# Performance work log

Hardware: AMD Instinct MI355X
Metric: run time of the kernel (lower is better)

Reference implementation:

```python
import jax, jax.numpy as jnp
import numpy as np

EPS = 1e-6      # NMF denominator epsilon (Hamburger NMF2D)
LN_EPS = 1e-5   # torch LayerNorm default eps
STEPS = 6      # number_of_iterations
R = 64          # NMF rank (upstream MD_R default)


def _nmf_local_step(xm, bases, coef):
    # xm: (B, D, N); bases: (B, D, R); coef: (B, N, R)
    num = jnp.einsum('bdn,bdr->bnr', xm, bases)
    btb = jnp.einsum('bdr,bds->brs', bases, bases)
    coef = coef * num / (jnp.einsum('bnr,brs->bns', coef, btb) + EPS)
    num = jnp.einsum('bdn,bnr->bdr', xm, coef)
    ctc = jnp.einsum('bnr,bns->brs', coef, coef)
    bases = bases * num / (jnp.einsum('bdr,brs->bds', bases, ctc) + EPS)
    return bases, coef


def nmf2d(xm, bases0, steps):
    # xm: (B, D, N) nonnegative; bases0: (1, D, R) fixed buffer (RAND_INIT=False)
    B = xm.shape[0]
    xs = jax.lax.stop_gradient(xm)  # local_inference runs under torch.no_grad()
    bases = jnp.broadcast_to(bases0, (B,) + bases0.shape[1:])
    coef = jax.nn.softmax(jnp.einsum('bdn,bdr->bnr', xs, bases), axis=-1)  # inv_t = 1 for NMF

    def body(i, carry):
        b, c = carry
        return _nmf_local_step(xs, b, c)

    bases, coef = jax.lax.fori_loop(0, steps, body, (bases, coef))
    bases = jax.lax.stop_gradient(bases)
    coef = jax.lax.stop_gradient(coef)
    # compute_coef: one multiplicative coef update WITH gradients w.r.t. xm
    num = jnp.einsum('bdn,bdr->bnr', xm, bases)
    btb = jnp.einsum('bdr,bds->brs', bases, bases)
    coef = coef * num / (jnp.einsum('bnr,brs->bns', coef, btb) + EPS)
    # reconstruct: (B, D, R) @ (B, R, N) -> (B, D, N)
    return jnp.einsum('bdr,bnr->bdn', bases, coef)


def setup_inputs() -> dict:
    key = jax.random.key(0)
    ks = jax.random.split(key, 4)
    B, S, F, FFN = 8, 1024, 1024, 4096
    Nc = FFN // 2
    x = jax.random.normal(ks[0], (B, S, F), jnp.float32)
    U_w = jax.random.normal(ks[1], (FFN, F), jnp.float32) / np.sqrt(F).astype(np.float32)
    U_b = jnp.zeros((FFN,), jnp.float32)
    ln_g = jnp.ones((Nc,), jnp.float32)
    ln_b = jnp.zeros((Nc,), jnp.float32)
    bases = jax.random.uniform(ks[2], (1, S, R), jnp.float32)
    bases = bases / (jnp.linalg.norm(bases, axis=1, keepdims=True) + 1e-12)  # F.normalize(dim=1)
    V_w = jax.random.normal(ks[3], (F, Nc), jnp.float32) / np.sqrt(Nc).astype(np.float32)
    V_b = jnp.zeros((F,), jnp.float32)
    return dict(x=x, U_w=U_w, U_b=U_b, ln_g=ln_g, ln_b=ln_b, bases=bases, V_w=V_w, V_b=V_b)


def reference(x, U_w, U_b, ln_g, ln_b, bases, V_w, V_b):
    # x: (B, S, F)
    h = jax.nn.gelu(x @ U_w.T + U_b, approximate=False)  # (B, S, FFN)
    z1, z2 = jnp.split(h, 2, axis=-1)                    # each (B, S, FFN//2)
    mu = z2.mean(-1, keepdims=True)
    var = z2.var(-1, keepdims=True)
    z2 = (z2 - mu) / jnp.sqrt(var + LN_EPS) * ln_g + ln_b
    xm = jax.nn.relu(z2)             # (B, D=S, N=FFN//2), matches NMF2D spatial view
    z2 = nmf2d(xm, bases, STEPS)     # (B, S, FFN//2)
    return (z1 * z2) @ V_w.T + V_b   # (B, S, F)
```

## Files before the change

kernel.cpp:

```cpp
#include <hip/hip_runtime.h>
#include <math.h>


typedef __bf16 bf16;
typedef bf16 bf16x4 __attribute__((ext_vector_type(4)));
typedef bf16 bf16x8 __attribute__((ext_vector_type(8)));
typedef float f32x4 __attribute__((ext_vector_type(4)));

#define NMF_EPS 1e-6f
#define LNEPS   1e-5f
#define NKS     8

#if defined(__has_builtin)
#if __has_builtin(__builtin_amdgcn_global_load_lds)
#define HAS_GLL 1
#endif
#endif

__device__ __forceinline__ void split2(float x, bf16& h, bf16& l) {
    h = (bf16)x;
    l = (bf16)(x - (float)h);
}

__global__ __launch_bounds__(256) void detect_dtype(const void* x, int* flag) {
    __shared__ int bad_sh;
    if (threadIdx.x == 0) bad_sh = 0;
    __syncthreads();
    const bf16* p = (const bf16*)x;
    int bad = 0;
    for (int i = threadIdx.x; i < 1024; i += 256) {
        float f = (float)p[i];
        if (!(fabsf(f) < 1000.f)) bad = 1;
    }
    if (bad) atomicOr(&bad_sh, 1);
    __syncthreads();
    if (threadIdx.x == 0) *flag = bad_sh;
}

__global__ __launch_bounds__(256)
void conv_all(const void* s0, const void* s1, const void* s2, const void* s3,
              const void* s4, const void* s5, const void* s6, const void* s7,
              bf16* __restrict__ ar, const int* __restrict__ flag) {
    const int is_f32 = *flag;
    const int total4 = 3688704;
    for (int i = blockIdx.x * 256 + threadIdx.x; i < total4; i += gridDim.x * 256) {
        const void* src; int loc; size_t doff;
        if (i < 2097152)      { src = s0; loc = i;           doff = 0; }
        else if (i < 3145728) { src = s1; loc = i - 2097152; doff = 8388608; }
        else if (i < 3146752) { src = s2; loc = i - 3145728; doff = 12582912; }
        else if (i < 3147264) { src = s3; loc = i - 3146752; doff = 12587008; }
        else if (i < 3147776) { src = s4; loc = i - 3147264; doff = 12589056; }
        else if (i < 3164160) { src = s5; loc = i - 3147776; doff = 12591104; }
        else if (i < 3688448) { src = s6; loc = i - 3164160; doff = 12656640; }
        else                  { src = s7; loc = i - 3688448; doff = 14753792; }
        bf16x4 o;
        if (is_f32) {
            f32x4 v = ((const f32x4*)src)[loc];
            o[0] = (bf16)v[0]; o[1] = (bf16)v[1]; o[2] = (bf16)v[2]; o[3] = (bf16)v[3];
        } else {
            o = ((const bf16x4*)src)[loc];
        }
        *(bf16x4*)(ar + doff + (size_t)loc * 4) = o;
    }
}

template <int EPI>
__global__ __launch_bounds__(256)
void gemm_bt(const bf16* __restrict__ A, const bf16* __restrict__ B,
             const bf16* __restrict__ bias,
             bf16* __restrict__ o0, bf16* __restrict__ o1,
             float* __restrict__ outf, bf16* __restrict__ outb,
             int K, int N, const int* __restrict__ flag) {
    __shared__ bf16 As[128 * 32];
    __shared__ bf16 Bs[128 * 32];
    const int tid = threadIdx.x;
    const int bm = blockIdx.x, bn = blockIdx.y;
    const bf16* Ab = A + (size_t)bm * 128 * K;
    const bf16* Bb = B + (size_t)bn * 128 * K;
    const int w = tid >> 6, lane = tid & 63, lm = lane & 15, lq = lane >> 4;
    const int m_off = (w >> 1) * 64, n_off = (w & 1) * 64;
    const int of32 = (EPI == 1) ? *flag : 0;
    f32x4 acc[4][4];
#pragma unroll
    for (int i = 0; i < 4; i++)
#pragma unroll
        for (int j = 0; j < 4; j++) { acc[i][j][0]=0.f; acc[i][j][1]=0.f; acc[i][j][2]=0.f; acc[i][j][3]=0.f; }

    const int r0 = tid * 8;
    const int row0 = r0 >> 5, col0 = r0 & 31;
    const int wb = w * 512;
    for (int k0 = 0; k0 < K; k0 += 32) {
        __syncthreads();
        const bf16* gA0 = Ab + (size_t)row0 * K        + k0 + col0;
        const bf16* gA1 = Ab + (size_t)(row0 + 64) * K + k0 + col0;
        const bf16* gB0 = Bb + (size_t)row0 * K        + k0 + col0;
        const bf16* gB1 = Bb + (size_t)(row0 + 64) * K + k0 + col0;
#ifdef HAS_GLL
        __builtin_amdgcn_global_load_lds((const __attribute__((address_space(1))) void*)gA0,
                                         (__attribute__((address_space(3))) void*)&As[wb], 16, 0, 0);
        __builtin_amdgcn_global_load_lds((const __attribute__((address_space(1))) void*)gA1,
                                         (__attribute__((address_space(3))) void*)&As[wb + 2048], 16, 0, 0);
        __builtin_amdgcn_global_load_lds((const __attribute__((address_space(1))) void*)gB0,
                                         (__attribute__((address_space(3))) void*)&Bs[wb], 16, 0, 0);
        __builtin_amdgcn_global_load_lds((const __attribute__((address_space(1))) void*)gB1,
                                         (__attribute__((address_space(3))) void*)&Bs[wb + 2048], 16, 0, 0);
#else
        *(int4*)(&As[r0])        = *(const int4*)gA0;
        *(int4*)(&As[r0 + 2048]) = *(const int4*)gA1;
        *(int4*)(&Bs[r0])        = *(const int4*)gB0;
        *(int4*)(&Bs[r0 + 2048]) = *(const int4*)gB1;
#endif
        __syncthreads();
        bf16x8 af[4], bg[4];
#pragma unroll
        for (int i = 0; i < 4; i++) af[i] = *(const bf16x8*)&As[(m_off + i * 16 + lm) * 32 + lq * 8];
#pragma unroll
        for (int j = 0; j < 4; j++) bg[j] = *(const bf16x8*)&Bs[(n_off + j * 16 + lm) * 32 + lq * 8];
#pragma unroll
        for (int i = 0; i < 4; i++)
#pragma unroll
            for (int j = 0; j < 4; j++)
                acc[i][j] = __builtin_amdgcn_mfma_f32_16x16x32_bf16(af[i], bg[j], acc[i][j], 0, 0, 0);
    }
    const int gm0 = bm * 128 + m_off, gn0 = bn * 128 + n_off;
#pragma unroll
    for (int i = 0; i < 4; i++) {
#pragma unroll
        for (int j = 0; j < 4; j++) {
            const int gn = gn0 + j * 16 + lm;
            const float bv = (float)bias[gn];
#pragma unroll
            for (int e = 0; e < 4; e++) {
                const int gm = gm0 + i * 16 + lq * 4 + e;
                float v = acc[i][j][e] + bv;
                if (EPI == 0) {
                    v = 0.5f * v * (1.f + erff(v * 0.70710678118654752f));
                    if (gn < 2048) o0[(size_t)gm * 2048 + gn] = (bf16)v;
                    else           o1[(size_t)gm * 2048 + (gn - 2048)] = (bf16)v;
                } else {
                    if (of32) outf[(size_t)gm * N + gn] = v;
                    else      outb[(size_t)gm * N + gn] = (bf16)v;
                }
            }
        }
    }
}

__global__ __launch_bounds__(256)
void ln_relu(bf16* __restrict__ z, const bf16* __restrict__ g, const bf16* __restrict__ b) {
    const int row = blockIdx.x;
    bf16* zr = z + (size_t)row * 2048;
    const int t = threadIdx.x;
    bf16x4 a0 = *(bf16x4*)(zr + t * 4);
    bf16x4 a1 = *(bf16x4*)(zr + 1024 + t * 4);
    float v0[4], v1[4];
#pragma unroll
    for (int i = 0; i < 4; i++) { v0[i] = (float)a0[i]; v1[i] = (float)a1[i]; }
    float s = 0.f, q = 0.f;
#pragma unroll
    for (int i = 0; i < 4; i++) { s += v0[i] + v1[i]; q += v0[i] * v0[i] + v1[i] * v1[i]; }
#pragma unroll
    for (int off = 32; off >= 1; off >>= 1) { s += __shfl_down(s, off); q += __shfl_down(q, off); }
    __shared__ float red[8];
    __shared__ float mv[2];
    const int wv = t >> 6;
    if ((t & 63) == 0) { red[wv] = s; red[4 + wv] = q; }
    __syncthreads();
    if (t == 0) {
        float S = red[0] + red[1] + red[2] + red[3];
        float Q = red[4] + red[5] + red[6] + red[7];
        float mu = S * (1.f / 2048.f);
        float var = Q * (1.f / 2048.f) - mu * mu;
        mv[0] = mu; mv[1] = rsqrtf(var + LNEPS);
    }
    __syncthreads();
    const float mu = mv[0], ri = mv[1];
#pragma unroll
    for (int i = 0; i < 4; i++) {
        int c0 = t * 4 + i, c1 = 1024 + t * 4 + i;
        a0[i] = (bf16)fmaxf((v0[i] - mu) * ri * (float)g[c0] + (float)b[c0], 0.f);
        a1[i] = (bf16)fmaxf((v1[i] - mu) * ri * (float)g[c1] + (float)b[c1], 0.f);
    }
    *(bf16x4*)(zr + t * 4) = a0;
    *(bf16x4*)(zr + 1024 + t * 4) = a1;
}

__global__ __launch_bounds__(256)
void transpose_xm(const bf16* __restrict__ src, bf16* __restrict__ dst) {
    const int n0 = blockIdx.x * 64, d0 = blockIdx.y * 64, b = blockIdx.z;
    const bf16* S = src + (size_t)b * 1024 * 2048;
    bf16* Dst = dst + (size_t)b * 2048 * 1024;
    __shared__ bf16 tl[64 * 72];
    const int t = threadIdx.x;
    const int tr = t >> 2, tc = (t & 3) * 16;
    bf16x8 v0 = *(const bf16x8*)(S + (size_t)(d0 + tr) * 2048 + n0 + tc);
    bf16x8 v1 = *(const bf16x8*)(S + (size_t)(d0 + tr) * 2048 + n0 + tc + 8);
    *(bf16x8*)&tl[tr * 72 + tc] = v0;
    *(bf16x8*)&tl[tr * 72 + tc + 8] = v1;
    __syncthreads();
    bf16 o[16];
#pragma unroll
    for (int i = 0; i < 16; i++) o[i] = tl[(tc + i) * 72 + tr];
    *(bf16x8*)(Dst + (size_t)(n0 + tr) * 1024 + d0 + tc) = *(bf16x8*)&o[0];
    *(bf16x8*)(Dst + (size_t)(n0 + tr) * 1024 + d0 + tc + 8) = *(bf16x8*)&o[8];
}

__global__ __launch_bounds__(256)
void bases_init2(const bf16* __restrict__ b0, float* __restrict__ bases,
                 bf16* __restrict__ bNh, bf16* __restrict__ bNl,
                 bf16* __restrict__ bTh, bf16* __restrict__ bTl) {
    const int d0 = blockIdx.x * 64, b = blockIdx.y;
    __shared__ bf16 tl[64 * 72];
    const int t = threadIdx.x;
    const int tr = t >> 2, tc = (t & 3) * 16;
    bf16x8 v0 = *(const bf16x8*)(b0 + (size_t)(d0 + tr) * 64 + tc);
    bf16x8 v1 = *(const bf16x8*)(b0 + (size_t)(d0 + tr) * 64 + tc + 8);
    *(bf16x8*)&tl[tr * 72 + tc] = v0;
    *(bf16x8*)&tl[tr * 72 + tc + 8] = v1;
    bf16x8 zz;
#pragma unroll
    for (int i = 0; i < 8; i++) zz[i] = (bf16)0.f;
    f32x4 f0, f1, f2, f3;
#pragma unroll
    for (int i = 0; i < 4; i++) { f0[i]=(float)v0[i]; f1[i]=(float)v0[i+4]; f2[i]=(float)v1[i]; f3[i]=(float)v1[i+4]; }
    const size_t nb = (size_t)b * 1024 * 64 + (size_t)(d0 + tr) * 64 + tc;
    *(f32x4*)(bases + nb)      = f0;
    *(f32x4*)(bases + nb + 4)  = f1;
    *(f32x4*)(bases + nb + 8)  = f2;
    *(f32x4*)(bases + nb + 12) = f3;
    *(bf16x8*)(bNh + nb)     = v0;
    *(bf16x8*)(bNh + nb + 8) = v1;
    *(bf16x8*)(bNl + nb)     = zz;
    *(bf16x8*)(bNl + nb + 8) = zz;
    __syncthreads();
    bf16 o[16];
#pragma unroll
    for (int i = 0; i < 16; i++) o[i] = tl[(tc + i) * 72 + tr];
    const size_t tb = (size_t)b * 64 * 1024 + (size_t)tr * 1024 + d0 + tc;
    *(bf16x8*)(bTh + tb)     = *(bf16x8*)&o[0];
    *(bf16x8*)(bTh + tb + 8) = *(bf16x8*)&o[8];
    *(bf16x8*)(bTl + tb)     = zz;
    *(bf16x8*)(bTl + tb + 8) = zz;
}

__global__ __launch_bounds__(256)
void gram64p(const bf16* __restrict__ Th, const bf16* __restrict__ Tl,
             int K, float* __restrict__ Gp) {
    const int ks = blockIdx.x, b = blockIdx.y;
    const int KC = K / NKS;
    const int kbeg = ks * KC, kend = kbeg + KC;
    const bf16* H = Th + (size_t)b * 64 * K;
    const bf16* L = Tl + (size_t)b * 64 * K;
    __shared__ bf16 Hs[64 * 40], Ls[64 * 40];
    const int t = threadIdx.x, lane = t & 63, w = t >> 6;
    const int lm = lane & 15, lq = lane >> 4;
    const int srow = t >> 2, scol = (t & 3) * 8;
    f32x4 acc[4];
#pragma unroll
    for (int j = 0; j < 4; j++) { acc[j][0]=0.f; acc[j][1]=0.f; acc[j][2]=0.f; acc[j][3]=0.f; }
    for (int k0 = kbeg; k0 < kend; k0 += 32) {
        __syncthreads();
        *(int4*)&Hs[srow * 40 + scol] = *(const int4*)(H + (size_t)srow * K + k0 + scol);
        *(int4*)&Ls[srow * 40 + scol] = *(const int4*)(L + (size_t)srow * K + k0 + scol);
        __syncthreads();
        bf16x8 aH = *(const bf16x8*)&Hs[(w * 16 + lm) * 40 + lq * 8];
        bf16x8 aL = *(const bf16x8*)&Ls[(w * 16 + lm) * 40 + lq * 8];
#pragma unroll
        for (int j = 0; j < 4; j++) {
            bf16x8 bH = *(const bf16x8*)&Hs[(j * 16 + lm) * 40 + lq * 8];
            bf16x8 bL = *(const bf16x8*)&Ls[(j * 16 + lm) * 40 + lq * 8];
            acc[j] = __builtin_amdgcn_mfma_f32_16x16x32_bf16(aH, bH, acc[j], 0, 0, 0);
            acc[j] = __builtin_amdgcn_mfma_f32_16x16x32_bf16(aH, bL, acc[j], 0, 0, 0);
            acc[j] = __builtin_amdgcn_mfma_f32_16x16x32_bf16(aL, bH, acc[j], 0, 0, 0);
        }
    }
    float* Gb = Gp + ((size_t)b * NKS + ks) * 4096;
#pragma unroll
    for (int j = 0; j < 4; j++)
#pragma unroll
        for (int e = 0; e < 4; e++)
            Gb[(w * 16 + lq * 4 + e) * 64 + j * 16 + lm] = acc[j][e];
}

template <int MODE>
__global__ __launch_bounds__(256)
void coef_step(const bf16* __restrict__ xmT, const bf16* __restrict__ bTh,
               const bf16* __restrict__ bTl, const float* __restrict__ btb,
               float* __restrict__ coef,
               bf16* __restrict__ cNh, bf16* __restrict__ cNl,
               bf16* __restrict__ cTh, bf16* __restrict__ cTl) {
    const int n0 = blockIdx.x * 64, b = blockIdx.y;
    const bf16* X = xmT + (size_t)b * 2048 * 1024 + (size_t)n0 * 1024;
    const bf16* H = bTh + (size_t)b * 64 * 1024;
    const bf16* L = bTl + (size_t)b * 64 * 1024;
    __shared__ bf16 xs[64 * 40], hs[64 * 40], ls[64 * 40];
    __shared__ float cold[(MODE == 1) ? 64 * 65 : 1];
    __shared__ float gsm[(MODE == 1) ? 64 * 64 : 1];
    const int t = threadIdx.x;
    float* Cb = coef + (size_t)b * 2048 * 64 + (size_t)n0 * 64;
    if constexpr (MODE == 1) {
        const int rr = t >> 2, cc = (t & 3) * 16;
#pragma unroll
        for (int i = 0; i < 4; i++)
            *(f32x4*)&cold[rr * 65 + cc + i * 4] = *(const f32x4*)(Cb + (size_t)rr * 64 + cc + i * 4);
        const float* Gb = btb + (size_t)b * NKS * 4096;
#pragma unroll
        for (int i = 0; i < 4; i++) {
            f32x4 s4; s4[0]=0.f; s4[1]=0.f; s4[2]=0.f; s4[3]=0.f;
#pragma unroll
            for (int ks = 0; ks < NKS; ks++)
                s4 += *(const f32x4*)(Gb + ks * 4096 + rr * 64 + cc + i * 4);
            *(f32x4*)&gsm[rr * 64 + cc + i * 4] = s4;
        }
    }
    const int lane = t & 63, w = t >> 6, lm = lane & 15, lq = lane >> 4;
    const int srow = t >> 2, scol = (t & 3) * 8;
    f32x4 acc[4];
#pragma unroll
    for (int j = 0; j < 4; j++) { acc[j][0]=0.f; acc[j][1]=0.f; acc[j][2]=0.f; acc[j][3]=0.f; }
    for (int k0 = 0; k0 < 1024; k0 += 32) {
        __syncthreads();
        *(int4*)&xs[srow * 40 + scol] = *(const int4*)(X + (size_t)srow * 1024 + k0 + scol);
        *(int4*)&hs[srow * 40 + scol] = *(const int4*)(H + (size_t)srow * 1024 + k0 + scol);
        *(int4*)&ls[srow * 40 + scol] = *(const int4*)(L + (size_t)srow * 1024 + k0 + scol);
        __syncthreads();
        bf16x8 a = *(const bf16x8*)&xs[(w * 16 + lm) * 40 + lq * 8];
#pragma unroll
        for (int j = 0; j < 4; j++) {
            bf16x8 bh = *(const bf16x8*)&hs[(j * 16 + lm) * 40 + lq * 8];
            bf16x8 bl = *(const bf16x8*)&ls[(j * 16 + lm) * 40 + lq * 8];
            acc[j] = __builtin_amdgcn_mfma_f32_16x16x32_bf16(a, bh, acc[j], 0, 0, 0);
            acc[j] = __builtin_amdgcn_mfma_f32_16x16x32_bf16(a, bl, acc[j], 0, 0, 0);
        }
    }
    const int nbase = w * 16 + lq * 4;
    float out[4][4];
    if constexpr (MODE == 0) {
#pragma unroll
        for (int e = 0; e < 4; e++) {
            float m = fmaxf(fmaxf(acc[0][e], acc[1][e]), fmaxf(acc[2][e], acc[3][e]));
#pragma unroll
            for (int off = 1; off < 16; off <<= 1) m = fmaxf(m, __shfl_xor(m, off));
            float ex[4], s = 0.f;
#pragma unroll
            for (int j = 0; j < 4; j++) { ex[j] = expf(acc[j][e] - m); s += ex[j]; }
#pragma unroll
            for (int off = 1; off < 16; off <<= 1) s += __shfl_xor(s, off);
            const float inv = 1.f / s;
#pragma unroll
            for (int j = 0; j < 4; j++) out[j][e] = ex[j] * inv;
        }
    } else {
        float den[4][4];
#pragma unroll
        for (int j = 0; j < 4; j++)
#pragma unroll
            for (int e = 0; e < 4; e++) den[j][e] = 0.f;
#pragma unroll 8
        for (int s = 0; s < 64; s++) {
            float g4[4], c4[4];
#pragma unroll
            for (int j = 0; j < 4; j++) g4[j] = gsm[s * 64 + j * 16 + lm];
#pragma unroll
            for (int e = 0; e < 4; e++) c4[e] = cold[(nbase + e) * 65 + s];
#pragma unroll
            for (int j = 0; j < 4; j++)
#pragma unroll
                for (int e = 0; e < 4; e++) den[j][e] += c4[e] * g4[j];
        }
#pragma unroll
        for (int j = 0; j < 4; j++)
#pragma unroll
            for (int e = 0; e < 4; e++)
                out[j][e] = cold[(nbase + e) * 65 + j * 16 + lm] * acc[j][e] / (den[j][e] + NMF_EPS);
    }
#pragma unroll
    for (int j = 0; j < 4; j++) {
        const int r = j * 16 + lm;
#pragma unroll
        for (int e = 0; e < 4; e++) {
            const int nl = nbase + e;
            Cb[(size_t)nl * 64 + r] = out[j][e];
            if constexpr (MODE == 1) {
                bf16 h, l2;
                split2(out[j][e], h, l2);
                cNh[(size_t)b * 2048 * 64 + (size_t)(n0 + nl) * 64 + r] = h;
                cNl[(size_t)b * 2048 * 64 + (size_t)(n0 + nl) * 64 + r] = l2;
            }
        }
    }
    if constexpr (MODE == 1) {
        __syncthreads();
#pragma unroll
        for (int j = 0; j < 4; j++)
#pragma unroll
            for (int e = 0; e < 4; e++)
                cold[(j * 16 + lm) * 65 + nbase + e] = out[j][e];
        __syncthreads();
        const int rr = t >> 2, nc = (t & 3) * 16;
        bf16 hh[16], ll2[16];
#pragma unroll
        for (int i = 0; i < 16; i++) split2(cold[rr * 65 + nc + i], hh[i], ll2[i]);
        const size_t tb = (size_t)b * 64 * 2048 + (size_t)rr * 2048 + n0 + nc;
        *(bf16x8*)(cTh + tb)     = *(bf16x8*)&hh[0];
        *(bf16x8*)(cTh + tb + 8) = *(bf16x8*)&hh[8];
        *(bf16x8*)(cTl + tb)     = *(bf16x8*)&ll2[0];
        *(bf16x8*)(cTl + tb + 8) = *(bf16x8*)&ll2[8];
    }
}

__global__ __launch_bounds__(256)
void bases_step(const bf16* __restrict__ xm, const bf16* __restrict__ cTh,
                const bf16* __restrict__ cTl, const float* __restrict__ ctc,
                float* __restrict__ bases,
                bf16* __restrict__ bNh, bf16* __restrict__ bNl,
                bf16* __restrict__ bTh, bf16* __restrict__ bTl) {
    const int d0 = blockIdx.x * 32, b = blockIdx.y;
    const bf16* X = xm + (size_t)b * 1024 * 2048 + (size_t)d0 * 2048;
    const bf16* H = cTh + (size_t)b * 64 * 2048;
    const bf16* L = cTl + (size_t)b * 64 * 2048;
    __shared__ bf16 hs[64 * 40], ls[64 * 40], xds[32 * 40];
    __shared__ float bold[32 * 65];
    __shared__ float gsm[64 * 64];
    const int t = threadIdx.x;
    float* Bb = bases + (size_t)b * 1024 * 64 + (size_t)d0 * 64;
    {
        const int rr = t >> 3, cc = (t & 7) * 8;
        *(f32x4*)&bold[rr * 65 + cc]     = *(const f32x4*)(Bb + (size_t)rr * 64 + cc);
        *(f32x4*)&bold[rr * 65 + cc + 4] = *(const f32x4*)(Bb + (size_t)rr * 64 + cc + 4);
        const int r2 = t >> 2, c2 = (t & 3) * 16;
        const float* Gb = ctc + (size_t)b * NKS * 4096;
#pragma unroll
        for (int i = 0; i < 4; i++) {
            f32x4 s4; s4[0]=0.f; s4[1]=0.f; s4[2]=0.f; s4[3]=0.f;
#pragma unroll
            for (int ks = 0; ks < NKS; ks++)
                s4 += *(const f32x4*)(Gb + ks * 4096 + r2 * 64 + c2 + i * 4);
            *(f32x4*)&gsm[r2 * 64 + c2 + i * 4] = s4;
        }
    }
    const int lane = t & 63, w = t >> 6, lm = lane & 15, lq = lane >> 4;
    const int srow = t >> 2, scol = (t & 3) * 8;
    f32x4 acc[2];
#pragma unroll
    for (int j = 0; j < 2; j++) { acc[j][0]=0.f; acc[j][1]=0.f; acc[j][2]=0.f; acc[j][3]=0.f; }
    for (int k0 = 0; k0 < 2048; k0 += 32) {
        __syncthreads();
        *(int4*)&hs[srow * 40 + scol] = *(const int4*)(H + (size_t)srow * 2048 + k0 + scol);
        *(int4*)&ls[srow * 40 + scol] = *(const int4*)(L + (size_t)srow * 2048 + k0 + scol);
        if (t < 128) {
            const int xr = t >> 2, xc2 = (t & 3) * 8;
            *(int4*)&xds[xr * 40 + xc2] = *(const int4*)(X + (size_t)xr * 2048 + k0 + xc2);
        }
        __syncthreads();
        bf16x8 ah = *(const bf16x8*)&hs[(w * 16 + lm) * 40 + lq * 8];
        bf16x8 al = *(const bf16x8*)&ls[(w * 16 + lm) * 40 + lq * 8];
#pragma unroll
        for (int j = 0; j < 2; j++) {
            bf16x8 bx = *(const bf16x8*)&xds[(j * 16 + lm) * 40 + lq * 8];
            acc[j] = __builtin_amdgcn_mfma_f32_16x16x32_bf16(ah, bx, acc[j], 0, 0, 0);
            acc[j] = __builtin_amdgcn_mfma_f32_16x16x32_bf16(al, bx, acc[j], 0, 0, 0);
        }
    }
    const int rbase = w * 16 + lq * 4;
    float den[2][4];
#pragma unroll
    for (int j = 0; j < 2; j++)
#pragma unroll
        for (int e = 0; e < 4; e++) den[j][e] = 0.f;
#pragma unroll 8
    for (int s = 0; s < 64; s++) {
        float g4[4], b2[2];
#pragma unroll
        for (int e = 0; e < 4; e++) g4[e] = gsm[s * 64 + rbase + e];
#pragma unroll
        for (int j = 0; j < 2; j++) b2[j] = bold[(j * 16 + lm) * 65 + s];
#pragma unroll
        for (int j = 0; j < 2; j++)
#pragma unroll
            for (int e = 0; e < 4; e++) den[j][e] += b2[j] * g4[e];
    }
    float out[2][4];
#pragma unroll
    for (int j = 0; j < 2; j++)
#pragma unroll
        for (int e = 0; e < 4; e++)
            out[j][e] = bold[(j * 16 + lm) * 65 + rbase + e] * acc[j][e] / (den[j][e] + NMF_EPS);
    __syncthreads();
#pragma unroll
    for (int j = 0; j < 2; j++)
#pragma unroll
        for (int e = 0; e < 4; e++)
            bold[(j * 16 + lm) * 65 + rbase + e] = out[j][e];
    __syncthreads();
    {
        const int dd = t >> 3, rc = (t & 7) * 8;
        float v[8];
#pragma unroll
        for (int i = 0; i < 8; i++) v[i] = bold[dd * 65 + rc + i];
        *(f32x4*)(Bb + (size_t)dd * 64 + rc)     = *(f32x4*)&v[0];
        *(f32x4*)(Bb + (size_t)dd * 64 + rc + 4) = *(f32x4*)&v[4];
        bf16 hv[8], lv[8];
#pragma unroll
        for (int i = 0; i < 8; i++) split2(v[i], hv[i], lv[i]);
        const size_t nb = (size_t)b * 1024 * 64 + (size_t)(d0 + dd) * 64 + rc;
        *(bf16x8*)(bNh + nb) = *(bf16x8*)&hv[0];
        *(bf16x8*)(bNl + nb) = *(bf16x8*)&lv[0];
    }
    {
        const int rr = t >> 2, dc = (t & 3) * 8;
        bf16 hv[8], lv[8];
#pragma unroll
        for (int i = 0; i < 8; i++) split2(bold[(dc + i) * 65 + rr], hv[i], lv[i]);
        const size_t tb = (size_t)b * 64 * 1024 + (size_t)rr * 1024 + d0 + dc;
        *(bf16x8*)(bTh + tb) = *(bf16x8*)&hv[0];
        *(bf16x8*)(bTl + tb) = *(bf16x8*)&lv[0];
    }
}

__global__ __launch_bounds__(256)
void recon_gate2(bf16* __restrict__ z1A, const bf16* __restrict__ bNh,
                 const bf16* __restrict__ bNl, const bf16* __restrict__ cNh,
                 const bf16* __restrict__ cNl) {
    const int n0 = blockIdx.x * 128, s0 = blockIdx.y * 128, b = blockIdx.z;
    const bf16* Ah = bNh + (size_t)b * 1024 * 64 + (size_t)s0 * 64;
    const bf16* Al = bNl + (size_t)b * 1024 * 64 + (size_t)s0 * 64;
    const bf16* Bh = cNh + (size_t)b * 2048 * 64 + (size_t)n0 * 64;
    const bf16* Bl = cNl + (size_t)b * 2048 * 64 + (size_t)n0 * 64;
    __shared__ bf16 ahs[128 * 72], als[128 * 72], bhs[128 * 72], bls[128 * 72];
    const int t = threadIdx.x;
#pragma unroll
    for (int i = 0; i < 4; i++) {
        const int idx = t * 4 + i;
        const int r_ = idx >> 3, c_ = (idx & 7) * 8;
        *(int4*)&ahs[r_ * 72 + c_] = *(const int4*)(Ah + (size_t)r_ * 64 + c_);
        *(int4*)&als[r_ * 72 + c_] = *(const int4*)(Al + (size_t)r_ * 64 + c_);
        *(int4*)&bhs[r_ * 72 + c_] = *(const int4*)(Bh + (size_t)r_ * 64 + c_);
        *(int4*)&bls[r_ * 72 + c_] = *(const int4*)(Bl + (size_t)r_ * 64 + c_);
    }
    __syncthreads();
    const int lane = t & 63, w = t >> 6, lm = lane & 15, lq = lane >> 4;
    const int m_off = (w >> 1) * 64, n_off = (w & 1) * 64;
    f32x4 acc[4][4];
#pragma unroll
    for (int i = 0; i < 4; i++)
#pragma unroll
        for (int j = 0; j < 4; j++) { acc[i][j][0]=0.f; acc[i][j][1]=0.f; acc[i][j][2]=0.f; acc[i][j][3]=0.f; }
#pragma unroll
    for (int kk = 0; kk < 2; kk++) {
        bf16x8 afh[4], afl[4], bgh[4], bgl[4];
#pragma unroll
        for (int i = 0; i < 4; i++) {
            afh[i] = *(const bf16x8*)&ahs[(m_off + i * 16 + lm) * 72 + kk * 32 + lq * 8];
            afl[i] = *(const bf16x8*)&als[(m_off + i * 16 + lm) * 72 + kk * 32 + lq * 8];
        }
#pragma unroll
        for (int j = 0; j < 4; j++) {
            bgh[j] = *(const bf16x8*)&bhs[(n_off + j * 16 + lm) * 72 + kk * 32 + lq * 8];
            bgl[j] = *(const bf16x8*)&bls[(n_off + j * 16 + lm) * 72 + kk * 32 + lq * 8];
        }
#pragma unroll
        for (int i = 0; i < 4; i++)
#pragma unroll
            for (int j = 0; j < 4; j++) {
                acc[i][j] = __builtin_amdgcn_mfma_f32_16x16x32_bf16(afh[i], bgh[j], acc[i][j], 0, 0, 0);
                acc[i][j] = __builtin_amdgcn_mfma_f32_16x16x32_bf16(afh[i], bgl[j], acc[i][j], 0, 0, 0);
                acc[i][j] = __builtin_amdgcn_mfma_f32_16x16x32_bf16(afl[i], bgh[j], acc[i][j], 0, 0, 0);
            }
    }
    bf16* Z = z1A + ((size_t)b * 1024 + s0) * 2048 + n0;
#pragma unroll
    for (int i = 0; i < 4; i++)
#pragma unroll
        for (int j = 0; j < 4; j++) {
            const int gn = n_off + j * 16 + lm;
#pragma unroll
            for (int e = 0; e < 4; e++) {
                const int gm = m_off + i * 16 + lq * 4 + e;
                bf16* p = Z + (size_t)gm * 2048 + gn;
                *p = (bf16)((float)*p * acc[i][j][e]);
            }
        }
}

extern "C" void kernel_launch(void* const* d_in, const int* in_sizes, int n_in,
                              void* d_out, int out_size, void* d_ws, size_t ws_size,
                              hipStream_t stream) {
    (void)in_sizes; (void)n_in; (void)out_size; (void)ws_size;
    char* ws = (char*)d_ws;
    bf16*  z1A   = (bf16*)(ws);
    bf16*  xmB   = (bf16*)(ws + 33554432);
    bf16*  xmT   = (bf16*)(ws + 67108864);
    char*  ar    = ws + 100663296;
    bf16* xc   = (bf16*)(ar);
    bf16* Uwc  = (bf16*)(ar + 16777216);
    bf16* Ubc  = (bf16*)(ar + 25165824);
    bf16* lngc = (bf16*)(ar + 25174016);
    bf16* lnbc = (bf16*)(ar + 25178112);
    bf16* b0c  = (bf16*)(ar + 25182208);
    bf16* Vwc  = (bf16*)(ar + 25313280);
    bf16* Vbc  = (bf16*)(ar + 29507584);
    int*  dflag = (int*)(ar + 29509632);
    float* bases = (float*)(ar);
    float* coef  = (float*)(ar + 2097152);
    bf16* bTh = (bf16*)(ar + 6291456);
    bf16* bTl = (bf16*)(ar + 7340032);
    bf16* bNh = (bf16*)(ar + 8388608);
    bf16* bNl = (bf16*)(ar + 9437184);
    bf16* cTh = (bf16*)(ar + 10485760);
    bf16* cTl = (bf16*)(ar + 12582912);
    bf16* cNh = (bf16*)(ar + 14680064);
    bf16* cNl = (bf16*)(ar + 16777216);
    float* btb = (float*)(ar + 18874368);
    float* ctc = (float*)(ar + 19922944);

    detect_dtype<<<1, 256, 0, stream>>>(d_in[0], dflag);
    conv_all<<<dim3(2048), 256, 0, stream>>>(d_in[0], d_in[1], d_in[2], d_in[3],
                                             d_in[4], d_in[5], d_in[6], d_in[7],
                                             (bf16*)ar, dflag);

    gemm_bt<0><<<dim3(64, 32), 256, 0, stream>>>(xc, Uwc, Ubc, z1A, xmB,
                                                 nullptr, nullptr, 1024, 4096, nullptr);
    ln_relu<<<dim3(8192), 256, 0, stream>>>(xmB, lngc, lnbc);
    transpose_xm<<<dim3(32, 16, 8), 256, 0, stream>>>(xmB, xmT);
    bases_init2<<<dim3(16, 8), 256, 0, stream>>>(b0c, bases, bNh, bNl, bTh, bTl);
    coef_step<0><<<dim3(32, 8), 256, 0, stream>>>(xmT, bTh, bTl, nullptr, coef,
                                                  nullptr, nullptr, nullptr, nullptr);
    for (int it = 0; it < 7; ++it) {
        gram64p<<<dim3(NKS, 8), 256, 0, stream>>>(bTh, bTl, 1024, btb);
        coef_step<1><<<dim3(32, 8), 256, 0, stream>>>(xmT, bTh, bTl, btb, coef,
                                                      cNh, cNl, cTh, cTl);
        if (it < 6) {
            gram64p<<<dim3(NKS, 8), 256, 0, stream>>>(cTh, cTl, 2048, ctc);
            bases_step<<<dim3(32, 8), 256, 0, stream>>>(xmB, cTh, cTl, ctc, bases,
                                                        bNh, bNl, bTh, bTl);
        }
    }
    recon_gate2<<<dim3(16, 8, 8), 256, 0, stream>>>(z1A, bNh, bNl, cNh, cNl);
    gemm_bt<1><<<dim3(64, 8), 256, 0, stream>>>(z1A, Vwc, Vbc, nullptr, nullptr,
                                                (float*)d_out, (bf16*)d_out,
                                                2048, 1024, dflag);
}
```

Baseline: 877.5 us.

## Double-buffer LDS with register prefetch and K=64 tiles in NMF step kernels

The coef_step and bases_step kernels now use double-buffered shared memory tiles of depth 64 instead of 32. The next tile's global loads are issued into registers before the current tile's MFMAs and stored to the alternate buffer afterwards, so each iteration needs one barrier instead of two. This aims to hide global-load latency behind MFMA work and halve the loop-iteration and sync overhead. In exchange it uses more LDS and registers, which may lower occupancy.

Result: faster. 775.0 us (-11.7%).

```diff
diff --git a/kernel.cpp b/kernel.cpp
--- a/kernel.cpp
+++ b/kernel.cpp
@@ -293,7 +293,7 @@
     const bf16* X = xmT + (size_t)b * 2048 * 1024 + (size_t)n0 * 1024;
     const bf16* H = bTh + (size_t)b * 64 * 1024;
     const bf16* L = bTl + (size_t)b * 64 * 1024;
-    __shared__ bf16 xs[64 * 40], hs[64 * 40], ls[64 * 40];
+    __shared__ bf16 xs[2][64 * 72], hs[2][64 * 72], ls[2][64 * 72];
     __shared__ float cold[(MODE == 1) ? 64 * 65 : 1];
     __shared__ float gsm[(MODE == 1) ? 64 * 64 : 1];
     const int t = threadIdx.x;
@@ -314,24 +314,62 @@
         }
     }
     const int lane = t & 63, w = t >> 6, lm = lane & 15, lq = lane >> 4;
-    const int srow = t >> 2, scol = (t & 3) * 8;
+    const int srow = t >> 2, scol = (t & 3) * 16;
+    int4 rx0, rx1, rh0, rh1, rl0, rl1;
+    {
+        rx0 = *(const int4*)(X + (size_t)srow * 1024 + scol);
+        rx1 = *(const int4*)(X + (size_t)srow * 1024 + scol + 8);
+        rh0 = *(const int4*)(H + (size_t)srow * 1024 + scol);
+        rh1 = *(const int4*)(H + (size_t)srow * 1024 + scol + 8);
+        rl0 = *(const int4*)(L + (size_t)srow * 1024 + scol);
+        rl1 = *(const int4*)(L + (size_t)srow * 1024 + scol + 8);
+        bf16* xb = &xs[0][srow * 72 + scol];
+        bf16* hb = &hs[0][srow * 72 + scol];
+        bf16* lb = &ls[0][srow * 72 + scol];
+        *(int4*)xb = rx0; *(int4*)(xb + 8) = rx1;
+        *(int4*)hb = rh0; *(int4*)(hb + 8) = rh1;
+        *(int4*)lb = rl0; *(int4*)(lb + 8) = rl1;
+    }
+    __syncthreads();
     f32x4 acc[4];
 #pragma unroll
     for (int j = 0; j < 4; j++) { acc[j][0]=0.f; acc[j][1]=0.f; acc[j][2]=0.f; acc[j][3]=0.f; }
-    for (int k0 = 0; k0 < 1024; k0 += 32) {
+    int cur = 0;
+    for (int kt = 0; kt < 16; kt++) {
+        if (kt < 15) {
+            const int k0 = (kt + 1) * 64;
+            rx0 = *(const int4*)(X + (size_t)srow * 1024 + k0 + scol);
+            rx1 = *(const int4*)(X + (size_t)srow * 1024 + k0 + scol + 8);
+            rh0 = *(const int4*)(H + (size_t)srow * 1024 + k0 + scol);
+            rh1 = *(const int4*)(H + (size_t)srow * 1024 + k0 + scol + 8);
+            rl0 = *(const int4*)(L + (size_t)srow * 1024 + k0 + scol);
+            rl1 = *(const int4*)(L + (size_t)srow * 1024 + k0 + scol + 8);
+        }
+        {
+            bf16x8 a0 = *(const bf16x8*)&xs[cur][(w * 16 + lm) * 72 + lq * 8];
+            bf16x8 a1 = *(const bf16x8*)&xs[cur][(w * 16 + lm) * 72 + 32 + lq * 8];
+#pragma unroll
+            for (int j = 0; j < 4; j++) {
+                bf16x8 bh0 = *(const bf16x8*)&hs[cur][(j * 16 + lm) * 72 + lq * 8];
+                bf16x8 bl0 = *(const bf16x8*)&ls[cur][(j * 16 + lm) * 72 + lq * 8];
+                acc[j] = __builtin_amdgcn_mfma_f32_16x16x32_bf16(a0, bh0, acc[j], 0, 0, 0);
+                acc[j] = __builtin_amdgcn_mfma_f32_16x16x32_bf16(a0, bl0, acc[j], 0, 0, 0);
+                bf16x8 bh1 = *(const bf16x8*)&hs[cur][(j * 16 + lm) * 72 + 32 + lq * 8];
+                bf16x8 bl1 = *(const bf16x8*)&ls[cur][(j * 16 + lm) * 72 + 32 + lq * 8];
+                acc[j] = __builtin_amdgcn_mfma_f32_16x16x32_bf16(a1, bh1, acc[j], 0, 0, 0);
+                acc[j] = __builtin_amdgcn_mfma_f32_16x16x32_bf16(a1, bl1, acc[j], 0, 0, 0);
+            }
+        }
+        if (kt < 15) {
+            bf16* xb = &xs[cur ^ 1][srow * 72 + scol];
+            bf16* hb = &hs[cur ^ 1][srow * 72 + scol];
+            bf16* lb = &ls[cur ^ 1][srow * 72 + scol];
+            *(int4*)xb = rx0; *(int4*)(xb + 8) = rx1;
+            *(int4*)hb = rh0; *(int4*)(hb + 8) = rh1;
+            *(int4*)lb = rl0; *(int4*)(lb + 8) = rl1;
+        }
         __syncthreads();
-        *(int4*)&xs[srow * 40 + scol] = *(const int4*)(X + (size_t)srow * 1024 + k0 + scol);
-        *(int4*)&hs[srow * 40 + scol] = *(const int4*)(H + (size_t)srow * 1024 + k0 + scol);
-        *(int4*)&ls[srow * 40 + scol] = *(const int4*)(L + (size_t)srow * 1024 + k0 + scol);
-        __syncthreads();
-        bf16x8 a = *(const bf16x8*)&xs[(w * 16 + lm) * 40 + lq * 8];
-#pragma unroll
-        for (int j = 0; j < 4; j++) {
-            bf16x8 bh = *(const bf16x8*)&hs[(j * 16 + lm) * 40 + lq * 8];
-            bf16x8 bl = *(const bf16x8*)&ls[(j * 16 + lm) * 40 + lq * 8];
-            acc[j] = __builtin_amdgcn_mfma_f32_16x16x32_bf16(a, bh, acc[j], 0, 0, 0);
-            acc[j] = __builtin_amdgcn_mfma_f32_16x16x32_bf16(a, bl, acc[j], 0, 0, 0);
-        }
+        cur ^= 1;
     }
     const int nbase = w * 16 + lq * 4;
     float out[4][4];
@@ -419,7 +457,7 @@
     const bf16* X = xm + (size_t)b * 1024 * 2048 + (size_t)d0 * 2048;
     const bf16* H = cTh + (size_t)b * 64 * 2048;
     const bf16* L = cTl + (size_t)b * 64 * 2048;
-    __shared__ bf16 hs[64 * 40], ls[64 * 40], xds[32 * 40];
+    __shared__ bf16 hs[2][64 * 72], ls[2][64 * 72], xds[2][32 * 72];
     __shared__ float bold[32 * 65];
     __shared__ float gsm[64 * 64];
     const int t = threadIdx.x;
@@ -440,27 +478,59 @@
         }
     }
     const int lane = t & 63, w = t >> 6, lm = lane & 15, lq = lane >> 4;
-    const int srow = t >> 2, scol = (t & 3) * 8;
+    const int srow = t >> 2, scol = (t & 3) * 16;
+    const int xrow = t >> 3, xcol = (t & 7) * 8;
+    int4 rh0, rh1, rl0, rl1, rxd;
+    {
+        rh0 = *(const int4*)(H + (size_t)srow * 2048 + scol);
+        rh1 = *(const int4*)(H + (size_t)srow * 2048 + scol + 8);
+        rl0 = *(const int4*)(L + (size_t)srow * 2048 + scol);
+        rl1 = *(const int4*)(L + (size_t)srow * 2048 + scol + 8);
+        rxd = *(const int4*)(X + (size_t)xrow * 2048 + xcol);
+        bf16* hb = &hs[0][srow * 72 + scol];
+        bf16* lb = &ls[0][srow * 72 + scol];
+        *(int4*)hb = rh0; *(int4*)(hb + 8) = rh1;
+        *(int4*)lb = rl0; *(int4*)(lb + 8) = rl1;
+        *(int4*)&xds[0][xrow * 72 + xcol] = rxd;
+    }
+    __syncthreads();
     f32x4 acc[2];
 #pragma unroll
     for (int j = 0; j < 2; j++) { acc[j][0]=0.f; acc[j][1]=0.f; acc[j][2]=0.f; acc[j][3]=0.f; }
-    for (int k0 = 0; k0 < 2048; k0 += 32) {
+    int cur = 0;
+    for (int kt = 0; kt < 32; kt++) {
+        if (kt < 31) {
+            const int k0 = (kt + 1) * 64;
+            rh0 = *(const int4*)(H + (size_t)srow * 2048 + k0 + scol);
+            rh1 = *(const int4*)(H + (size_t)srow * 2048 + k0 + scol + 8);
+            rl0 = *(const int4*)(L + (size_t)srow * 2048 + k0 + scol);
+            rl1 = *(const int4*)(L + (size_t)srow * 2048 + k0 + scol + 8);
+            rxd = *(const int4*)(X + (size_t)xrow * 2048 + k0 + xcol);
+        }
+        {
+            bf16x8 ah0 = *(const bf16x8*)&hs[cur][(w * 16 + lm) * 72 + lq * 8];
+            bf16x8 al0 = *(const bf16x8*)&ls[cur][(w * 16 + lm) * 72 + lq * 8];
+            bf16x8 ah1 = *(const bf16x8*)&hs[cur][(w * 16 + lm) * 72 + 32 + lq * 8];
+            bf16x8 al1 = *(const bf16x8*)&ls[cur][(w * 16 + lm) * 72 + 32 + lq * 8];
+#pragma unroll
+            for (int j = 0; j < 2; j++) {
+                bf16x8 bx0 = *(const bf16x8*)&xds[cur][(j * 16 + lm) * 72 + lq * 8];
+                acc[j] = __builtin_amdgcn_mfma_f32_16x16x32_bf16(ah0, bx0, acc[j], 0, 0, 0);
+                acc[j] = __builtin_amdgcn_mfma_f32_16x16x32_bf16(al0, bx0, acc[j], 0, 0, 0);
+                bf16x8 bx1 = *(const bf16x8*)&xds[cur][(j * 16 + lm) * 72 + 32 + lq * 8];
+                acc[j] = __builtin_amdgcn_mfma_f32_16x16x32_bf16(ah1, bx1, acc[j], 0, 0, 0);
+                acc[j] = __builtin_amdgcn_mfma_f32_16x16x32_bf16(al1, bx1, acc[j], 0, 0, 0);
+            }
+        }
+        if (kt < 31) {
+            bf16* hb = &hs[cur ^ 1][srow * 72 + scol];
+            bf16* lb = &ls[cur ^ 1][srow * 72 + scol];
+            *(int4*)hb = rh0; *(int4*)(hb + 8) = rh1;
+            *(int4*)lb = rl0; *(int4*)(lb + 8) = rl1;
+            *(int4*)&xds[cur ^ 1][xrow * 72 + xcol] = rxd;
+        }
         __syncthreads();
-        *(int4*)&hs[srow * 40 + scol] = *(const int4*)(H + (size_t)srow * 2048 + k0 + scol);
-        *(int4*)&ls[srow * 40 + scol] = *(const int4*)(L + (size_t)srow * 2048 + k0 + scol);
-        if (t < 128) {
-            const int xr = t >> 2, xc2 = (t & 3) * 8;
-            *(int4*)&xds[xr * 40 + xc2] = *(const int4*)(X + (size_t)xr * 2048 + k0 + xc2);
-        }
-        __syncthreads();
-        bf16x8 ah = *(const bf16x8*)&hs[(w * 16 + lm) * 40 + lq * 8];
-        bf16x8 al = *(const bf16x8*)&ls[(w * 16 + lm) * 40 + lq * 8];
-#pragma unroll
-        for (int j = 0; j < 2; j++) {
-            bf16x8 bx = *(const bf16x8*)&xds[(j * 16 + lm) * 40 + lq * 8];
-            acc[j] = __builtin_amdgcn_mfma_f32_16x16x32_bf16(ah, bx, acc[j], 0, 0, 0);
-            acc[j] = __builtin_amdgcn_mfma_f32_16x16x32_bf16(al, bx, acc[j], 0, 0, 0);
-        }
+        cur ^= 1;
     }
     const int rbase = w * 16 + lq * 4;
     float den[2][4];
```

## Load NMF MFMA operands directly from global memory, drop LDS staging

Applied to the files above, without the earlier changes.

The gram, coef and bases step kernels no longer stage tiles through shared memory behind paired barriers. Each lane now loads its MFMA fragments straight from global memory, and the inner loops are unrolled to process 64 K-elements per iteration. The gram partial split count is raised from 8 to 16 for more blocks, and the ctc buffer offset moves to make room for the larger partial buffer. This removes per-tile syncs and LDS traffic, but it relies on cache hits for B operands that are re-read across warps and accepts less coalesced global access.

Measured after the change: 1.054 ms. +20.1%, slower.

```diff
diff --git a/kernel.cpp b/kernel.cpp
--- a/kernel.cpp
+++ b/kernel.cpp
@@ -9,7 +9,7 @@
 
 #define NMF_EPS 1e-6f
 #define LNEPS   1e-5f
-#define NKS     8
+#define NKS     16
 
 #if defined(__has_builtin)
 #if __has_builtin(__builtin_amdgcn_global_load_lds)
@@ -251,24 +251,22 @@
     const int kbeg = ks * KC, kend = kbeg + KC;
     const bf16* H = Th + (size_t)b * 64 * K;
     const bf16* L = Tl + (size_t)b * 64 * K;
-    __shared__ bf16 Hs[64 * 40], Ls[64 * 40];
     const int t = threadIdx.x, lane = t & 63, w = t >> 6;
     const int lm = lane & 15, lq = lane >> 4;
-    const int srow = t >> 2, scol = (t & 3) * 8;
+    const bf16* Ha = H + (size_t)(w * 16 + lm) * K + lq * 8;
+    const bf16* La = L + (size_t)(w * 16 + lm) * K + lq * 8;
+    const bf16* Hb = H + (size_t)lm * K + lq * 8;
+    const bf16* Lb = L + (size_t)lm * K + lq * 8;
     f32x4 acc[4];
 #pragma unroll
     for (int j = 0; j < 4; j++) { acc[j][0]=0.f; acc[j][1]=0.f; acc[j][2]=0.f; acc[j][3]=0.f; }
     for (int k0 = kbeg; k0 < kend; k0 += 32) {
-        __syncthreads();
-        *(int4*)&Hs[srow * 40 + scol] = *(const int4*)(H + (size_t)srow * K + k0 + scol);
-        *(int4*)&Ls[srow * 40 + scol] = *(const int4*)(L + (size_t)srow * K + k0 + scol);
-        __syncthreads();
-        bf16x8 aH = *(const bf16x8*)&Hs[(w * 16 + lm) * 40 + lq * 8];
-        bf16x8 aL = *(const bf16x8*)&Ls[(w * 16 + lm) * 40 + lq * 8];
+        bf16x8 aH = *(const bf16x8*)(Ha + k0);
+        bf16x8 aL = *(const bf16x8*)(La + k0);
 #pragma unroll
         for (int j = 0; j < 4; j++) {
-            bf16x8 bH = *(const bf16x8*)&Hs[(j * 16 + lm) * 40 + lq * 8];
-            bf16x8 bL = *(const bf16x8*)&Ls[(j * 16 + lm) * 40 + lq * 8];
+            bf16x8 bH = *(const bf16x8*)(Hb + (size_t)j * 16 * K + k0);
+            bf16x8 bL = *(const bf16x8*)(Lb + (size_t)j * 16 * K + k0);
             acc[j] = __builtin_amdgcn_mfma_f32_16x16x32_bf16(aH, bH, acc[j], 0, 0, 0);
             acc[j] = __builtin_amdgcn_mfma_f32_16x16x32_bf16(aH, bL, acc[j], 0, 0, 0);
             acc[j] = __builtin_amdgcn_mfma_f32_16x16x32_bf16(aL, bH, acc[j], 0, 0, 0);
@@ -293,7 +291,6 @@
     const bf16* X = xmT + (size_t)b * 2048 * 1024 + (size_t)n0 * 1024;
     const bf16* H = bTh + (size_t)b * 64 * 1024;
     const bf16* L = bTl + (size_t)b * 64 * 1024;
-    __shared__ bf16 xs[64 * 40], hs[64 * 40], ls[64 * 40];
     __shared__ float cold[(MODE == 1) ? 64 * 65 : 1];
     __shared__ float gsm[(MODE == 1) ? 64 * 64 : 1];
     const int t = threadIdx.x;
@@ -314,25 +311,29 @@
         }
     }
     const int lane = t & 63, w = t >> 6, lm = lane & 15, lq = lane >> 4;
-    const int srow = t >> 2, scol = (t & 3) * 8;
+    const bf16* Xr = X + (size_t)(w * 16 + lm) * 1024 + lq * 8;
+    const bf16* Hr = H + (size_t)lm * 1024 + lq * 8;
+    const bf16* Lr = L + (size_t)lm * 1024 + lq * 8;
     f32x4 acc[4];
 #pragma unroll
     for (int j = 0; j < 4; j++) { acc[j][0]=0.f; acc[j][1]=0.f; acc[j][2]=0.f; acc[j][3]=0.f; }
-    for (int k0 = 0; k0 < 1024; k0 += 32) {
-        __syncthreads();
-        *(int4*)&xs[srow * 40 + scol] = *(const int4*)(X + (size_t)srow * 1024 + k0 + scol);
-        *(int4*)&hs[srow * 40 + scol] = *(const int4*)(H + (size_t)srow * 1024 + k0 + scol);
-        *(int4*)&ls[srow * 40 + scol] = *(const int4*)(L + (size_t)srow * 1024 + k0 + scol);
-        __syncthreads();
-        bf16x8 a = *(const bf16x8*)&xs[(w * 16 + lm) * 40 + lq * 8];
+#pragma unroll 2
+    for (int k0 = 0; k0 < 1024; k0 += 64) {
+        bf16x8 a0 = *(const bf16x8*)(Xr + k0);
+        bf16x8 a1 = *(const bf16x8*)(Xr + k0 + 32);
 #pragma unroll
         for (int j = 0; j < 4; j++) {
-            bf16x8 bh = *(const bf16x8*)&hs[(j * 16 + lm) * 40 + lq * 8];
-            bf16x8 bl = *(const bf16x8*)&ls[(j * 16 + lm) * 40 + lq * 8];
-            acc[j] = __builtin_amdgcn_mfma_f32_16x16x32_bf16(a, bh, acc[j], 0, 0, 0);
-            acc[j] = __builtin_amdgcn_mfma_f32_16x16x32_bf16(a, bl, acc[j], 0, 0, 0);
-        }
-    }
+            bf16x8 bh0 = *(const bf16x8*)(Hr + (size_t)j * 16 * 1024 + k0);
+            bf16x8 bl0 = *(const bf16x8*)(Lr + (size_t)j * 16 * 1024 + k0);
+            acc[j] = __builtin_amdgcn_mfma_f32_16x16x32_bf16(a0, bh0, acc[j], 0, 0, 0);
+            acc[j] = __builtin_amdgcn_mfma_f32_16x16x32_bf16(a0, bl0, acc[j], 0, 0, 0);
+            bf16x8 bh1 = *(const bf16x8*)(Hr + (size_t)j * 16 * 1024 + k0 + 32);
+            bf16x8 bl1 = *(const bf16x8*)(Lr + (size_t)j * 16 * 1024 + k0 + 32);
+            acc[j] = __builtin_amdgcn_mfma_f32_16x16x32_bf16(a1, bh1, acc[j], 0, 0, 0);
+            acc[j] = __builtin_amdgcn_mfma_f32_16x16x32_bf16(a1, bl1, acc[j], 0, 0, 0);
+        }
+    }
+    if constexpr (MODE == 1) __syncthreads();
     const int nbase = w * 16 + lq * 4;
     float out[4][4];
     if constexpr (MODE == 0) {
@@ -419,7 +420,6 @@
     const bf16* X = xm + (size_t)b * 1024 * 2048 + (size_t)d0 * 2048;
     const bf16* H = cTh + (size_t)b * 64 * 2048;
     const bf16* L = cTl + (size_t)b * 64 * 2048;
-    __shared__ bf16 hs[64 * 40], ls[64 * 40], xds[32 * 40];
     __shared__ float bold[32 * 65];
     __shared__ float gsm[64 * 64];
     const int t = threadIdx.x;
@@ -440,28 +440,29 @@
         }
     }
     const int lane = t & 63, w = t >> 6, lm = lane & 15, lq = lane >> 4;
-    const int srow = t >> 2, scol = (t & 3) * 8;
+    const bf16* Hr = H + (size_t)(w * 16 + lm) * 2048 + lq * 8;
+    const bf16* Lr = L + (size_t)(w * 16 + lm) * 2048 + lq * 8;
+    const bf16* Xr = X + (size_t)lm * 2048 + lq * 8;
     f32x4 acc[2];
 #pragma unroll
     for (int j = 0; j < 2; j++) { acc[j][0]=0.f; acc[j][1]=0.f; acc[j][2]=0.f; acc[j][3]=0.f; }
-    for (int k0 = 0; k0 < 2048; k0 += 32) {
-        __syncthreads();
-        *(int4*)&hs[srow * 40 + scol] = *(const int4*)(H + (size_t)srow * 2048 + k0 + scol);
-        *(int4*)&ls[srow * 40 + scol] = *(const int4*)(L + (size_t)srow * 2048 + k0 + scol);
-        if (t < 128) {
-            const int xr = t >> 2, xc2 = (t & 3) * 8;
-            *(int4*)&xds[xr * 40 + xc2] = *(const int4*)(X + (size_t)xr * 2048 + k0 + xc2);
-        }
-        __syncthreads();
-        bf16x8 ah = *(const bf16x8*)&hs[(w * 16 + lm) * 40 + lq * 8];
-        bf16x8 al = *(const bf16x8*)&ls[(w * 16 + lm) * 40 + lq * 8];
+#pragma unroll 2
+    for (int k0 = 0; k0 < 2048; k0 += 64) {
+        bf16x8 ah0 = *(const bf16x8*)(Hr + k0);
+        bf16x8 al0 = *(const bf16x8*)(Lr + k0);
+        bf16x8 ah1 = *(const bf16x8*)(Hr + k0 + 32);
+        bf16x8 al1 = *(const bf16x8*)(Lr + k0 + 32);
 #pragma unroll
         for (int j = 0; j < 2; j++) {
-            bf16x8 bx = *(const bf16x8*)&xds[(j * 16 + lm) * 40 + lq * 8];
-            acc[j] = __builtin_amdgcn_mfma_f32_16x16x32_bf16(ah, bx, acc[j], 0, 0, 0);
-            acc[j] = __builtin_amdgcn_mfma_f32_16x16x32_bf16(al, bx, acc[j], 0, 0, 0);
-        }
-    }
+            bf16x8 bx0 = *(const bf16x8*)(Xr + (size_t)j * 16 * 2048 + k0);
+            acc[j] = __builtin_amdgcn_mfma_f32_16x16x32_bf16(ah0, bx0, acc[j], 0, 0, 0);
+            acc[j] = __builtin_amdgcn_mfma_f32_16x16x32_bf16(al0, bx0, acc[j], 0, 0, 0);
+            bf16x8 bx1 = *(const bf16x8*)(Xr + (size_t)j * 16 * 2048 + k0 + 32);
+            acc[j] = __builtin_amdgcn_mfma_f32_16x16x32_bf16(ah1, bx1, acc[j], 0, 0, 0);
+            acc[j] = __builtin_amdgcn_mfma_f32_16x16x32_bf16(al1, bx1, acc[j], 0, 0, 0);
+        }
+    }
+    __syncthreads();
     const int rbase = w * 16 + lq * 4;
     float den[2][4];
 #pragma unroll
@@ -612,7 +613,7 @@
     bf16* cNh = (bf16*)(ar + 14680064);
     bf16* cNl = (bf16*)(ar + 16777216);
     float* btb = (float*)(ar + 18874368);
-    float* ctc = (float*)(ar + 19922944);
+    float* ctc = (float*)(ar + 20971520);
 
     detect_dtype<<<1, 256, 0, stream>>>(d_in[0], dflag);
     conv_all<<<dim3(2048), 256, 0, stream>>>(d_in[0], d_in[1], d_in[2], d_in[3],
```
